# Optimization experiments

Measured on AMD Instinct MI355X. Metric: run time of the kernel, lower is better.

## Reference

```python
import jax, jax.numpy as jnp
import numpy as np

BATCH, IN, OUT, G = 2048, 512, 512, 8


def setup_inputs() -> dict:
    key = jax.random.key(0)
    k1, k2, k3 = jax.random.split(key, 3)
    x = jax.random.normal(k1, (BATCH, IN), dtype=jnp.float32)
    # spline coefficients, initialized small like normal_(c, 0, 0.001)
    c = jax.random.normal(k2, (G, OUT, IN), dtype=jnp.float32) * 0.001
    # residual weights, xavier-like small init
    w_b = jax.random.normal(k3, (OUT, IN), dtype=jnp.float32) * 0.001
    w_s = jnp.ones((OUT, IN), dtype=jnp.float32)
    # RBF grid centers over [-2, 2] (get_size() == G)
    grid = jnp.arange(G, dtype=jnp.float32) * (4.0 / (G - 1)) - 2.0
    return {"x": x, "c": c, "w_b": w_b, "w_s": w_s, "grid": grid}


def _basis(x, grid):
    # Gaussian RBF basis: [batch, G, in]
    d = x[:, None, :] - grid[None, :, None]
    return jnp.exp(-(d * d))


def reference(x, c, w_b, w_s, grid):
    basis_vals = _basis(x, grid)                      # [b, n=G, i]
    # faithful to th.einsum('bni,aoi->boi', ...): n and a are independently summed
    spline_out = jnp.einsum('bni,aoi->boi', basis_vals, c)  # [b, o, i]
    spline_out = spline_out * w_s[None]
    res_out = jax.nn.silu(x)[:, None, :] * w_b[None]  # [b, o, i]
    return (spline_out + res_out).sum(axis=-1)        # [b, o]
```

## Files before the change

### kernel.cpp

```cpp
#include <hip/hip_runtime.h>

#define BATCH 2048
#define IN    512
#define OUT   512
#define NG    8
#define KTOT  1024

#define BM 64
#define BN 32
#define BK 64
#define PAD 88
#define NIT (KTOT / BK)

typedef __attribute__((ext_vector_type(8))) short bf16x8;
typedef __attribute__((ext_vector_type(4))) float f32x4;

__device__ inline unsigned short f2bf(float f) {
    union { float f; unsigned int u; } v; v.f = f;
    unsigned int r = v.u + 0x7fffu + ((v.u >> 16) & 1u);
    return (unsigned short)(r >> 16);
}

__global__ __launch_bounds__(256) void prep_kernel(const float* __restrict__ x,
                                                   const float* __restrict__ c,
                                                   const float* __restrict__ w_b,
                                                   const float* __restrict__ w_s,
                                                   const float* __restrict__ grid,
                                                   unsigned short* __restrict__ A,
                                                   unsigned short* __restrict__ B) {
    int blk = blockIdx.x;
    int tid = threadIdx.x;
    if (blk < 512) {
        int e = (blk * 256 + tid) * 8;
        float g[NG];
#pragma unroll
        for (int n = 0; n < NG; ++n) g[n] = grid[n];
        float4 x0 = *(const float4*)&x[e];
        float4 x1 = *(const float4*)&x[e + 4];
        float xv[8] = {x0.x, x0.y, x0.z, x0.w, x1.x, x1.y, x1.z, x1.w};
        unsigned short sv[8], lv[8];
#pragma unroll
        for (int j = 0; j < 8; ++j) {
            float s = 0.f;
#pragma unroll
            for (int n = 0; n < NG; ++n) { float d = xv[j] - g[n]; s += __expf(-d * d); }
            sv[j] = f2bf(s);
            lv[j] = f2bf(xv[j] / (1.f + __expf(-xv[j])));
        }
        int b = e >> 9, i = e & 511;
        *(int4*)&A[b * KTOT + i]       = *(int4*)sv;
        *(int4*)&A[b * KTOT + 512 + i] = *(int4*)lv;
    } else {
        int e = ((blk - 512) * 256 + tid) * 8;
        float acc[8] = {};
#pragma unroll
        for (int a = 0; a < NG; ++a) {
            float4 c0 = *(const float4*)&c[(size_t)a * (OUT * IN) + e];
            float4 c1 = *(const float4*)&c[(size_t)a * (OUT * IN) + e + 4];
            acc[0] += c0.x; acc[1] += c0.y; acc[2] += c0.z; acc[3] += c0.w;
            acc[4] += c1.x; acc[5] += c1.y; acc[6] += c1.z; acc[7] += c1.w;
        }
        float4 s0 = *(const float4*)&w_s[e];
        float4 s1 = *(const float4*)&w_s[e + 4];
        float sw[8] = {s0.x, s0.y, s0.z, s0.w, s1.x, s1.y, s1.z, s1.w};
        float4 b0 = *(const float4*)&w_b[e];
        float4 b1 = *(const float4*)&w_b[e + 4];
        float bw[8] = {b0.x, b0.y, b0.z, b0.w, b1.x, b1.y, b1.z, b1.w};
        unsigned short cv[8], bv[8];
#pragma unroll
        for (int j = 0; j < 8; ++j) { cv[j] = f2bf(acc[j] * sw[j]); bv[j] = f2bf(bw[j]); }
        int o = e >> 9, i = e & 511;
        *(int4*)&B[o * KTOT + i]       = *(int4*)cv;
        *(int4*)&B[o * KTOT + 512 + i] = *(int4*)bv;
    }
}

__global__ __launch_bounds__(256) void gemm_kernel(const unsigned short* __restrict__ A,
                                                   const unsigned short* __restrict__ B,
                                                   float* __restrict__ outp) {
    __shared__ short As[2][BM * PAD];
    __shared__ short Bs[2][BN * PAD];

    int tid  = threadIdx.x;
    int lane = tid & 63;
    int w    = tid >> 6;
    int wm   = w >> 1, wn = w & 1;
    int lr   = lane & 15, lg = lane >> 4;
    int m0   = blockIdx.y * BM;
    int n0   = blockIdx.x * BN;

    int srow = tid >> 3;
    int sc8  = tid & 7;

    const int4* Ag0 = (const int4*)&A[(size_t)(m0 + srow)      * KTOT + sc8 * 8];
    const int4* Ag1 = (const int4*)&A[(size_t)(m0 + srow + 32) * KTOT + sc8 * 8];
    const int4* Bg  = (const int4*)&B[(size_t)(n0 + srow)      * KTOT + sc8 * 8];

    int woA0 = srow * PAD + sc8 * 8;
    int woA1 = (srow + 32) * PAD + sc8 * 8;
    int woB  = srow * PAD + sc8 * 8;

    f32x4 acc0 = {0.f, 0.f, 0.f, 0.f};
    f32x4 acc1 = {0.f, 0.f, 0.f, 0.f};

    int4 ca0 = Ag0[0], ca1 = Ag1[0], cb = Bg[0];
    *(int4*)&As[0][woA0] = ca0;
    *(int4*)&As[0][woA1] = ca1;
    *(int4*)&Bs[0][woB]  = cb;
    ca0 = Ag0[8]; ca1 = Ag1[8]; cb = Bg[8];
    __syncthreads();

#pragma unroll
    for (int it = 0; it < NIT; ++it) {
        int cur = it & 1;
        if (it + 1 < NIT) {
            *(int4*)&As[cur ^ 1][woA0] = ca0;
            *(int4*)&As[cur ^ 1][woA1] = ca1;
            *(int4*)&Bs[cur ^ 1][woB]  = cb;
            if (it + 2 < NIT) {
                ca0 = Ag0[(it + 2) * 8]; ca1 = Ag1[(it + 2) * 8]; cb = Bg[(it + 2) * 8];
            }
        }
#pragma unroll
        for (int ks = 0; ks < 2; ++ks) {
            bf16x8 a0 = *(const bf16x8*)&As[cur][(wm * 32 + lr)      * PAD + ks * 32 + lg * 8];
            bf16x8 a1 = *(const bf16x8*)&As[cur][(wm * 32 + 16 + lr) * PAD + ks * 32 + lg * 8];
            bf16x8 b  = *(const bf16x8*)&Bs[cur][(wn * 16 + lr)      * PAD + ks * 32 + lg * 8];
            acc0 = __builtin_amdgcn_mfma_f32_16x16x32_bf16(a0, b, acc0, 0, 0, 0);
            acc1 = __builtin_amdgcn_mfma_f32_16x16x32_bf16(a1, b, acc1, 0, 0, 0);
        }
        __syncthreads();
    }

    int orow = m0 + wm * 32 + lg * 4;
    int ocol = n0 + wn * 16 + lr;
#pragma unroll
    for (int r = 0; r < 4; ++r) {
        outp[(size_t)(orow + r) * OUT + ocol]      = acc0[r];
        outp[(size_t)(orow + 16 + r) * OUT + ocol] = acc1[r];
    }
}

extern "C" void kernel_launch(void* const* d_in, const int* in_sizes, int n_in,
                              void* d_out, int out_size, void* d_ws, size_t ws_size,
                              hipStream_t stream) {
    (void)in_sizes; (void)n_in; (void)out_size; (void)ws_size;
    const float* x    = (const float*)d_in[0];
    const float* c    = (const float*)d_in[1];
    const float* w_b  = (const float*)d_in[2];
    const float* w_s  = (const float*)d_in[3];
    const float* grid = (const float*)d_in[4];
    float* outp = (float*)d_out;

    unsigned short* A = (unsigned short*)d_ws;
    unsigned short* B = A + (size_t)BATCH * KTOT;

    prep_kernel<<<512 + 128, 256, 0, stream>>>(x, c, w_b, w_s, grid, A, B);
    gemm_kernel<<<dim3(OUT / BN, BATCH / BM), 256, 0, stream>>>(A, B, outp);
}
```

Measured before the change: 19.87 us.

## Use 64x64 GEMM tiles with 512 threads, swizzled block order, cheaper RBF sum

The GEMM tile grows to 64x64 with 8 waves per block, each wave now computing 16x32 and reusing one A fragment across two B fragments. Blocks use a 1D grid remapped so neighbouring blocks share A and B tiles in cache. Separately, the RBF basis sum replaces eight exps per element with two exps plus a Horner polynomial, which assumes a uniformly spaced grid. This halves block count and cuts exp work, but gives fewer blocks for occupancy and relies on the grid being evenly spaced.

```diff
diff --git a/kernel.cpp b/kernel.cpp
--- a/kernel.cpp
+++ b/kernel.cpp
@@ -7,7 +7,7 @@
 #define KTOT  1024
 
 #define BM 64
-#define BN 32
+#define BN 64
 #define BK 64
 #define PAD 88
 #define NIT (KTOT / BK)
@@ -32,19 +32,25 @@
     int tid = threadIdx.x;
     if (blk < 512) {
         int e = (blk * 256 + tid) * 8;
-        float g[NG];
+        float g0 = grid[0];
+        float dl = grid[1] - g0;
+        float d2 = dl * dl;
+        float dn[NG];
 #pragma unroll
-        for (int n = 0; n < NG; ++n) g[n] = grid[n];
+        for (int n = 0; n < NG; ++n) dn[n] = __expf(-d2 * (float)(n * n));
         float4 x0 = *(const float4*)&x[e];
         float4 x1 = *(const float4*)&x[e + 4];
         float xv[8] = {x0.x, x0.y, x0.z, x0.w, x1.x, x1.y, x1.z, x1.w};
         unsigned short sv[8], lv[8];
 #pragma unroll
         for (int j = 0; j < 8; ++j) {
-            float s = 0.f;
+            float u  = xv[j] - g0;
+            float e1 = __expf(-u * u);
+            float q  = __expf(2.f * dl * u);
+            float p  = dn[NG - 1];
 #pragma unroll
-            for (int n = 0; n < NG; ++n) { float d = xv[j] - g[n]; s += __expf(-d * d); }
-            sv[j] = f2bf(s);
+            for (int n = NG - 2; n >= 0; --n) p = p * q + dn[n];
+            sv[j] = f2bf(e1 * p);
             lv[j] = f2bf(xv[j] / (1.f + __expf(-xv[j])));
         }
         int b = e >> 9, i = e & 511;
@@ -75,7 +81,7 @@
     }
 }
 
-__global__ __launch_bounds__(256) void gemm_kernel(const unsigned short* __restrict__ A,
+__global__ __launch_bounds__(512) void gemm_kernel(const unsigned short* __restrict__ A,
                                                    const unsigned short* __restrict__ B,
                                                    float* __restrict__ outp) {
     __shared__ short As[2][BM * PAD];
@@ -86,58 +92,57 @@
     int w    = tid >> 6;
     int wm   = w >> 1, wn = w & 1;
     int lr   = lane & 15, lg = lane >> 4;
-    int m0   = blockIdx.y * BM;
-    int n0   = blockIdx.x * BN;
+
+    int bid  = blockIdx.x;
+    int mg   = bid & 7;
+    int rest = bid >> 3;
+    int sub  = rest >> 3;
+    int ncol = rest & 7;
+    int m0   = (mg * 4 + sub) * BM;
+    int n0   = ncol * BN;
 
     int srow = tid >> 3;
     int sc8  = tid & 7;
 
-    const int4* Ag0 = (const int4*)&A[(size_t)(m0 + srow)      * KTOT + sc8 * 8];
-    const int4* Ag1 = (const int4*)&A[(size_t)(m0 + srow + 32) * KTOT + sc8 * 8];
-    const int4* Bg  = (const int4*)&B[(size_t)(n0 + srow)      * KTOT + sc8 * 8];
+    const int4* Ag = (const int4*)&A[(size_t)(m0 + srow) * KTOT + sc8 * 8];
+    const int4* Bg = (const int4*)&B[(size_t)(n0 + srow) * KTOT + sc8 * 8];
 
-    int woA0 = srow * PAD + sc8 * 8;
-    int woA1 = (srow + 32) * PAD + sc8 * 8;
-    int woB  = srow * PAD + sc8 * 8;
+    int wo = srow * PAD + sc8 * 8;
 
     f32x4 acc0 = {0.f, 0.f, 0.f, 0.f};
     f32x4 acc1 = {0.f, 0.f, 0.f, 0.f};
 
-    int4 ca0 = Ag0[0], ca1 = Ag1[0], cb = Bg[0];
-    *(int4*)&As[0][woA0] = ca0;
-    *(int4*)&As[0][woA1] = ca1;
-    *(int4*)&Bs[0][woB]  = cb;
-    ca0 = Ag0[8]; ca1 = Ag1[8]; cb = Bg[8];
+    int4 ca = Ag[0], cb = Bg[0];
+    *(int4*)&As[0][wo] = ca;
+    *(int4*)&Bs[0][wo] = cb;
+    ca = Ag[8]; cb = Bg[8];
     __syncthreads();
 
 #pragma unroll
     for (int it = 0; it < NIT; ++it) {
         int cur = it & 1;
         if (it + 1 < NIT) {
-            *(int4*)&As[cur ^ 1][woA0] = ca0;
-            *(int4*)&As[cur ^ 1][woA1] = ca1;
-            *(int4*)&Bs[cur ^ 1][woB]  = cb;
-            if (it + 2 < NIT) {
-                ca0 = Ag0[(it + 2) * 8]; ca1 = Ag1[(it + 2) * 8]; cb = Bg[(it + 2) * 8];
-            }
+            *(int4*)&As[cur ^ 1][wo] = ca;
+            *(int4*)&Bs[cur ^ 1][wo] = cb;
+            if (it + 2 < NIT) { ca = Ag[(it + 2) * 8]; cb = Bg[(it + 2) * 8]; }
         }
 #pragma unroll
         for (int ks = 0; ks < 2; ++ks) {
-            bf16x8 a0 = *(const bf16x8*)&As[cur][(wm * 32 + lr)      * PAD + ks * 32 + lg * 8];
-            bf16x8 a1 = *(const bf16x8*)&As[cur][(wm * 32 + 16 + lr) * PAD + ks * 32 + lg * 8];
-            bf16x8 b  = *(const bf16x8*)&Bs[cur][(wn * 16 + lr)      * PAD + ks * 32 + lg * 8];
-            acc0 = __builtin_amdgcn_mfma_f32_16x16x32_bf16(a0, b, acc0, 0, 0, 0);
-            acc1 = __builtin_amdgcn_mfma_f32_16x16x32_bf16(a1, b, acc1, 0, 0, 0);
+            bf16x8 a  = *(const bf16x8*)&As[cur][(wm * 16 + lr)      * PAD + ks * 32 + lg * 8];
+            bf16x8 b0 = *(const bf16x8*)&Bs[cur][(wn * 32 + lr)      * PAD + ks * 32 + lg * 8];
+            bf16x8 b1 = *(const bf16x8*)&Bs[cur][(wn * 32 + 16 + lr) * PAD + ks * 32 + lg * 8];
+            acc0 = __builtin_amdgcn_mfma_f32_16x16x32_bf16(a, b0, acc0, 0, 0, 0);
+            acc1 = __builtin_amdgcn_mfma_f32_16x16x32_bf16(a, b1, acc1, 0, 0, 0);
         }
         __syncthreads();
     }
 
-    int orow = m0 + wm * 32 + lg * 4;
-    int ocol = n0 + wn * 16 + lr;
+    int orow = m0 + wm * 16 + lg * 4;
+    int ocol = n0 + wn * 32 + lr;
 #pragma unroll
     for (int r = 0; r < 4; ++r) {
         outp[(size_t)(orow + r) * OUT + ocol]      = acc0[r];
-        outp[(size_t)(orow + 16 + r) * OUT + ocol] = acc1[r];
+        outp[(size_t)(orow + r) * OUT + ocol + 16] = acc1[r];
     }
 }
 
@@ -156,5 +161,5 @@
     unsigned short* B = A + (size_t)BATCH * KTOT;
 
     prep_kernel<<<512 + 128, 256, 0, stream>>>(x, c, w_b, w_s, grid, A, B);
-    gemm_kernel<<<dim3(OUT / BN, BATCH / BM), 256, 0, stream>>>(A, B, outp);
+    gemm_kernel<<<(BATCH / BM) * (OUT / BN), 512, 0, stream>>>(A, B, outp);
 }
```

Result: faster. 17.73 us (-10.8%).
